# Performance work log

Measured on AMD Instinct MI355X. Metric: run time of the kernel, lower is better.

## Reference

```python
import jax, jax.numpy as jnp
import numpy as np

B, T, I, H = 512, 1024, 64, 128

def setup_inputs() -> dict:
    key = jax.random.key(0)
    ks = jax.random.split(key, 7)
    s_ih = 1.0 / np.sqrt(H)  # torch nn.RNN init scale (uniform +-1/sqrt(H)); use scaled normal for stability
    return {
        "x": jax.random.normal(ks[0], (B, T, I), dtype=jnp.float32),
        "W_ih": jax.random.uniform(ks[1], (H, I), minval=-s_ih, maxval=s_ih, dtype=jnp.float32),
        "W_hh": jax.random.uniform(ks[2], (H, H), minval=-s_ih, maxval=s_ih, dtype=jnp.float32),
        "b_ih": jax.random.uniform(ks[3], (H,), minval=-s_ih, maxval=s_ih, dtype=jnp.float32),
        "b_hh": jax.random.uniform(ks[4], (H,), minval=-s_ih, maxval=s_ih, dtype=jnp.float32),
        "fc_w": jax.random.uniform(ks[5], (1, H), minval=-s_ih, maxval=s_ih, dtype=jnp.float32),
        "fc_b": jax.random.uniform(ks[6], (1,), minval=-s_ih, maxval=s_ih, dtype=jnp.float32),
    }

def reference(x, W_ih, W_hh, b_ih, b_hh, fc_w, fc_b):
    # Precompute input projection for all timesteps in one big GEMM: [B,T,H]
    xp = jnp.einsum("bti,hi->bth", x, W_ih) + b_ih + b_hh
    h0 = jnp.zeros((x.shape[0], W_hh.shape[0]), dtype=x.dtype)

    def step(h, xp_t):
        h = jnp.tanh(xp_t + h @ W_hh.T)
        return h, None

    # scan over time axis; only the final hidden state is needed (out[:, -1, :])
    h_last, _ = jax.lax.scan(step, h0, jnp.swapaxes(xp, 0, 1))
    out = h_last @ fc_w.T + fc_b  # [B, 1]
    return jax.nn.sigmoid(out)
```

## Files before the change

### kernel.cpp

```cpp
#include <hip/hip_runtime.h>


#define Bsz 512
#define Tt  1024
#define Ii  64
#define Hh  128
constexpr int TC = 32;
constexpr int NT = 256;

typedef _Float16 half2v __attribute__((ext_vector_type(2)));
typedef _Float16 half4v __attribute__((ext_vector_type(4)));
typedef _Float16 half8v __attribute__((ext_vector_type(8)));

union h8u { half8v v; half2v h[4]; };

__device__ __forceinline__ float dot2(half2v a, half2v b, float c) {
#if __has_builtin(__builtin_amdgcn_fdot2)
    return __builtin_amdgcn_fdot2(a, b, c, false);
#else
    return c + (float)a[0] * (float)b[0] + (float)a[1] * (float)b[1];
#endif
}

__device__ __forceinline__ float fast_tanh(float x) {
    float t = __builtin_amdgcn_exp2f(x * 2.8853900817779268f);
    return 1.0f - 2.0f * __builtin_amdgcn_rcpf(t + 1.0f);
}
__device__ __forceinline__ float fast_sigmoid(float z) {
    float t = __builtin_amdgcn_exp2f(-z * 1.4426950408889634f);
    return __builtin_amdgcn_rcpf(1.0f + t);
}
__device__ __forceinline__ half4v cvt4(float4 p) {
    half4v r; r[0] = (_Float16)p.x; r[1] = (_Float16)p.y;
    r[2] = (_Float16)p.z; r[3] = (_Float16)p.w; return r;
}

__global__ __launch_bounds__(NT, 4)
void rnn_fused(const float* __restrict__ x,
               const float* __restrict__ W_ih,
               const float* __restrict__ W_hh,
               const float* __restrict__ b_ih,
               const float* __restrict__ b_hh,
               const float* __restrict__ fc_w,
               const float* __restrict__ fc_b,
               float* __restrict__ out)
{
    __shared__ __align__(16) _Float16 xs[2][TC * Ii];
    __shared__ __align__(16) _Float16 hbuf[2][Hh];
    __shared__ float wred[NT / 64];

    const int tid = threadIdx.x;
    const int kq  = tid & 3;
    const int jg  = tid >> 2;
    const int j0  = jg * 2, j1 = j0 + 1;
    const int row = blockIdx.x;

    half2v wih0[8], wih1[8];
    {
        const float* g0 = W_ih + j0 * Ii + kq * 16;
        const float* g1 = W_ih + j1 * Ii + kq * 16;
        #pragma unroll
        for (int k = 0; k < 8; ++k) {
            wih0[k][0] = (_Float16)g0[2*k]; wih0[k][1] = (_Float16)g0[2*k+1];
            wih1[k][0] = (_Float16)g1[2*k]; wih1[k][1] = (_Float16)g1[2*k+1];
        }
    }
    half2v whh0[16], whh1[16];
    {
        const float* g0 = W_hh + j0 * Hh + kq * 32;
        const float* g1 = W_hh + j1 * Hh + kq * 32;
        #pragma unroll
        for (int k = 0; k < 16; ++k) {
            whh0[k][0] = (_Float16)g0[2*k]; whh0[k][1] = (_Float16)g0[2*k+1];
            whh1[k][0] = (_Float16)g1[2*k]; whh1[k][1] = (_Float16)g1[2*k+1];
        }
    }
    const float bias0 = b_ih[j0] + b_hh[j0];
    const float bias1 = b_ih[j1] + b_hh[j1];
    const float fw0 = fc_w[j0], fw1 = fc_w[j1];

    if (tid < Hh / 2) ((half2v*)hbuf[0])[tid] = (half2v)0;

    const float4* xsrc = (const float4*)(x + (size_t)row * Tt * Ii);
    float4 p0 = xsrc[tid];
    float4 p1 = xsrc[tid + NT];

    int   cur = 0;
    float h0n = 0.0f, h1n = 0.0f;

    for (int t0 = 0; t0 < Tt; t0 += TC) {
        const int cbuf = (t0 / TC) & 1;
        ((half4v*)xs[cbuf])[tid]      = cvt4(p0);
        ((half4v*)xs[cbuf])[tid + NT] = cvt4(p1);
        if (t0 + TC < Tt) {
            const int base = (t0 + TC) * (Ii / 4);
            p0 = xsrc[base + tid];
            p1 = xsrc[base + tid + NT];
        }
        __syncthreads();

        #pragma unroll 2
        for (int tt = 0; tt < TC; ++tt) {
            const half8v* xv = (const half8v*)(xs[cbuf] + tt * Ii) + kq * 2;
            const half8v* hv = (const half8v*)(hbuf[cur]) + kq * 4;
            h8u xq0, xq1, hq0, hq1, hq2, hq3;
            xq0.v = xv[0]; xq1.v = xv[1];
            hq0.v = hv[0]; hq1.v = hv[1];
            hq2.v = hv[2]; hq3.v = hv[3];

            float a0 = 0.f, a1 = 0.f, a2 = 0.f, a3 = 0.f;
            float c0 = 0.f, c1 = 0.f, c2 = 0.f, c3 = 0.f;
            #pragma unroll
            for (int k = 0; k < 4; ++k) {
                half2v u0 = xq0.h[k], u1 = xq1.h[k];
                a0 = dot2(u0, wih0[k],     a0);
                a1 = dot2(u1, wih0[k + 4], a1);
                c0 = dot2(u0, wih1[k],     c0);
                c1 = dot2(u1, wih1[k + 4], c1);
            }
            #pragma unroll
            for (int k = 0; k < 4; ++k) {
                half2v v0 = hq0.h[k], v1 = hq1.h[k];
                half2v v2 = hq2.h[k], v3 = hq3.h[k];
                a0 = dot2(v0, whh0[k],      a0);
                a1 = dot2(v1, whh0[k + 4],  a1);
                a2 = dot2(v2, whh0[k + 8],  a2);
                a3 = dot2(v3, whh0[k + 12], a3);
                c0 = dot2(v0, whh1[k],      c0);
                c1 = dot2(v1, whh1[k + 4],  c1);
                c2 = dot2(v2, whh1[k + 8],  c2);
                c3 = dot2(v3, whh1[k + 12], c3);
            }
            float pp0 = (a0 + a1) + (a2 + a3);
            float pp1 = (c0 + c1) + (c2 + c3);
            pp0 += __shfl_xor(pp0, 1, 64);
            pp0 += __shfl_xor(pp0, 2, 64);
            pp1 += __shfl_xor(pp1, 1, 64);
            pp1 += __shfl_xor(pp1, 2, 64);
            h0n = fast_tanh(pp0 + bias0);
            h1n = fast_tanh(pp1 + bias1);
            if (kq == 0) {
                half2v hw; hw[0] = (_Float16)h0n; hw[1] = (_Float16)h1n;
                ((half2v*)hbuf[cur ^ 1])[jg] = hw;
            }
            __syncthreads();
            cur ^= 1;
        }
    }

    float partial = (kq == 0) ? (fw0 * h0n + fw1 * h1n) : 0.0f;
    #pragma unroll
    for (int off = 32; off > 0; off >>= 1)
        partial += __shfl_down(partial, off, 64);
    if ((tid & 63) == 0) wred[tid >> 6] = partial;
    __syncthreads();
    if (tid == 0) {
        float z = fc_b[0];
        #pragma unroll
        for (int w = 0; w < NT / 64; ++w) z += wred[w];
        out[row] = fast_sigmoid(z);
    }
}

extern "C" void kernel_launch(void* const* d_in, const int* in_sizes, int n_in,
                              void* d_out, int out_size, void* d_ws, size_t ws_size,
                              hipStream_t stream) {
    const float* x    = (const float*)d_in[0];
    const float* W_ih = (const float*)d_in[1];
    const float* W_hh = (const float*)d_in[2];
    const float* b_ih = (const float*)d_in[3];
    const float* b_hh = (const float*)d_in[4];
    const float* fc_w = (const float*)d_in[5];
    const float* fc_b = (const float*)d_in[6];
    float* out = (float*)d_out;

    rnn_fused<<<Bsz, NT, 0, stream>>>(x, W_ih, W_hh, b_ih, b_hh, fc_w, fc_b, out);
}
```

Before: 625.5 us.

## Run each batch row's recurrence in a single wavefront without barriers

```diff
diff --git a/kernel.cpp b/kernel.cpp
--- a/kernel.cpp
+++ b/kernel.cpp
@@ -6,7 +6,7 @@
 #define Ii  64
 #define Hh  128
 constexpr int TC = 32;
-constexpr int NT = 256;
+constexpr int NT = 64;
 
 typedef _Float16 half2v __attribute__((ext_vector_type(2)));
 typedef _Float16 half4v __attribute__((ext_vector_type(4)));
@@ -35,42 +35,39 @@
     r[2] = (_Float16)p.z; r[3] = (_Float16)p.w; return r;
 }
 
-__global__ __launch_bounds__(NT, 4)
-void rnn_fused(const float* __restrict__ x,
-               const float* __restrict__ W_ih,
-               const float* __restrict__ W_hh,
-               const float* __restrict__ b_ih,
-               const float* __restrict__ b_hh,
-               const float* __restrict__ fc_w,
-               const float* __restrict__ fc_b,
-               float* __restrict__ out)
+__global__ __launch_bounds__(NT, 1)
+void rnn_wave(const float* __restrict__ x,
+              const float* __restrict__ W_ih,
+              const float* __restrict__ W_hh,
+              const float* __restrict__ b_ih,
+              const float* __restrict__ b_hh,
+              const float* __restrict__ fc_w,
+              const float* __restrict__ fc_b,
+              float* __restrict__ out)
 {
     __shared__ __align__(16) _Float16 xs[2][TC * Ii];
-    __shared__ __align__(16) _Float16 hbuf[2][Hh];
-    __shared__ float wred[NT / 64];
+    __shared__ __align__(16) _Float16 hs[Hh];
 
-    const int tid = threadIdx.x;
-    const int kq  = tid & 3;
-    const int jg  = tid >> 2;
-    const int j0  = jg * 2, j1 = j0 + 1;
+    const int L   = threadIdx.x;
     const int row = blockIdx.x;
+    const int j0  = 2 * L, j1 = j0 + 1;
 
-    half2v wih0[8], wih1[8];
+    half2v wih0[Ii / 2], wih1[Ii / 2];
     {
-        const float* g0 = W_ih + j0 * Ii + kq * 16;
-        const float* g1 = W_ih + j1 * Ii + kq * 16;
+        const float* g0 = W_ih + j0 * Ii;
+        const float* g1 = W_ih + j1 * Ii;
         #pragma unroll
-        for (int k = 0; k < 8; ++k) {
+        for (int k = 0; k < Ii / 2; ++k) {
             wih0[k][0] = (_Float16)g0[2*k]; wih0[k][1] = (_Float16)g0[2*k+1];
             wih1[k][0] = (_Float16)g1[2*k]; wih1[k][1] = (_Float16)g1[2*k+1];
         }
     }
-    half2v whh0[16], whh1[16];
+    half2v whh0[Hh / 2], whh1[Hh / 2];
     {
-        const float* g0 = W_hh + j0 * Hh + kq * 32;
-        const float* g1 = W_hh + j1 * Hh + kq * 32;
+        const float* g0 = W_hh + j0 * Hh;
+        const float* g1 = W_hh + j1 * Hh;
         #pragma unroll
-        for (int k = 0; k < 16; ++k) {
+        for (int k = 0; k < Hh / 2; ++k) {
             whh0[k][0] = (_Float16)g0[2*k]; whh0[k][1] = (_Float16)g0[2*k+1];
             whh1[k][0] = (_Float16)g1[2*k]; whh1[k][1] = (_Float16)g1[2*k+1];
         }
@@ -79,87 +76,70 @@
     const float bias1 = b_ih[j1] + b_hh[j1];
     const float fw0 = fc_w[j0], fw1 = fc_w[j1];
 
-    if (tid < Hh / 2) ((half2v*)hbuf[0])[tid] = (half2v)0;
+    ((half2v*)hs)[L] = (half2v)0;
 
     const float4* xsrc = (const float4*)(x + (size_t)row * Tt * Ii);
-    float4 p0 = xsrc[tid];
-    float4 p1 = xsrc[tid + NT];
+    float4 p[8];
+    #pragma unroll
+    for (int i = 0; i < 8; ++i) p[i] = xsrc[L + 64 * i];
 
-    int   cur = 0;
     float h0n = 0.0f, h1n = 0.0f;
 
     for (int t0 = 0; t0 < Tt; t0 += TC) {
         const int cbuf = (t0 / TC) & 1;
-        ((half4v*)xs[cbuf])[tid]      = cvt4(p0);
-        ((half4v*)xs[cbuf])[tid + NT] = cvt4(p1);
+        #pragma unroll
+        for (int i = 0; i < 8; ++i)
+            ((half4v*)xs[cbuf])[L + 64 * i] = cvt4(p[i]);
         if (t0 + TC < Tt) {
             const int base = (t0 + TC) * (Ii / 4);
-            p0 = xsrc[base + tid];
-            p1 = xsrc[base + tid + NT];
+            #pragma unroll
+            for (int i = 0; i < 8; ++i) p[i] = xsrc[base + L + 64 * i];
         }
-        __syncthreads();
 
-        #pragma unroll 2
+        #pragma unroll 1
         for (int tt = 0; tt < TC; ++tt) {
-            const half8v* xv = (const half8v*)(xs[cbuf] + tt * Ii) + kq * 2;
-            const half8v* hv = (const half8v*)(hbuf[cur]) + kq * 4;
-            h8u xq0, xq1, hq0, hq1, hq2, hq3;
-            xq0.v = xv[0]; xq1.v = xv[1];
-            hq0.v = hv[0]; hq1.v = hv[1];
-            hq2.v = hv[2]; hq3.v = hv[3];
+            const half8v* xv = (const half8v*)(xs[cbuf] + tt * Ii);
+            const half8v* hv = (const half8v*)hs;
 
             float a0 = 0.f, a1 = 0.f, a2 = 0.f, a3 = 0.f;
             float c0 = 0.f, c1 = 0.f, c2 = 0.f, c3 = 0.f;
+
             #pragma unroll
-            for (int k = 0; k < 4; ++k) {
-                half2v u0 = xq0.h[k], u1 = xq1.h[k];
-                a0 = dot2(u0, wih0[k],     a0);
-                a1 = dot2(u1, wih0[k + 4], a1);
-                c0 = dot2(u0, wih1[k],     c0);
-                c1 = dot2(u1, wih1[k + 4], c1);
+            for (int i = 0; i < 8; ++i) {
+                h8u q; q.v = xv[i];
+                a0 = dot2(q.h[0], wih0[4*i+0], a0);
+                a1 = dot2(q.h[1], wih0[4*i+1], a1);
+                a2 = dot2(q.h[2], wih0[4*i+2], a2);
+                a3 = dot2(q.h[3], wih0[4*i+3], a3);
+                c0 = dot2(q.h[0], wih1[4*i+0], c0);
+                c1 = dot2(q.h[1], wih1[4*i+1], c1);
+                c2 = dot2(q.h[2], wih1[4*i+2], c2);
+                c3 = dot2(q.h[3], wih1[4*i+3], c3);
             }
             #pragma unroll
-            for (int k = 0; k < 4; ++k) {
-                half2v v0 = hq0.h[k], v1 = hq1.h[k];
-                half2v v2 = hq2.h[k], v3 = hq3.h[k];
-                a0 = dot2(v0, whh0[k],      a0);
-                a1 = dot2(v1, whh0[k + 4],  a1);
-                a2 = dot2(v2, whh0[k + 8],  a2);
-                a3 = dot2(v3, whh0[k + 12], a3);
-                c0 = dot2(v0, whh1[k],      c0);
-                c1 = dot2(v1, whh1[k + 4],  c1);
-                c2 = dot2(v2, whh1[k + 8],  c2);
-                c3 = dot2(v3, whh1[k + 12], c3);
+            for (int i = 0; i < 16; ++i) {
+                h8u q; q.v = hv[i];
+                a0 = dot2(q.h[0], whh0[4*i+0], a0);
+                a1 = dot2(q.h[1], whh0[4*i+1], a1);
+                a2 = dot2(q.h[2], whh0[4*i+2], a2);
+                a3 = dot2(q.h[3], whh0[4*i+3], a3);
+                c0 = dot2(q.h[0], whh1[4*i+0], c0);
+                c1 = dot2(q.h[1], whh1[4*i+1], c1);
+                c2 = dot2(q.h[2], whh1[4*i+2], c2);
+                c3 = dot2(q.h[3], whh1[4*i+3], c3);
             }
-            float pp0 = (a0 + a1) + (a2 + a3);
-            float pp1 = (c0 + c1) + (c2 + c3);
-            pp0 += __shfl_xor(pp0, 1, 64);
-            pp0 += __shfl_xor(pp0, 2, 64);
-            pp1 += __shfl_xor(pp1, 1, 64);
-            pp1 += __shfl_xor(pp1, 2, 64);
-            h0n = fast_tanh(pp0 + bias0);
-            h1n = fast_tanh(pp1 + bias1);
-            if (kq == 0) {
-                half2v hw; hw[0] = (_Float16)h0n; hw[1] = (_Float16)h1n;
-                ((half2v*)hbuf[cur ^ 1])[jg] = hw;
-            }
-            __syncthreads();
-            cur ^= 1;
+            h0n = fast_tanh(((a0 + a1) + (a2 + a3)) + bias0);
+            h1n = fast_tanh(((c0 + c1) + (c2 + c3)) + bias1);
+            half2v hw; hw[0] = (_Float16)h0n; hw[1] = (_Float16)h1n;
+            ((half2v*)hs)[L] = hw;
         }
     }
 
-    float partial = (kq == 0) ? (fw0 * h0n + fw1 * h1n) : 0.0f;
+    float partial = fw0 * h0n + fw1 * h1n;
     #pragma unroll
     for (int off = 32; off > 0; off >>= 1)
         partial += __shfl_down(partial, off, 64);
-    if ((tid & 63) == 0) wred[tid >> 6] = partial;
-    __syncthreads();
-    if (tid == 0) {
-        float z = fc_b[0];
-        #pragma unroll
-        for (int w = 0; w < NT / 64; ++w) z += wred[w];
-        out[row] = fast_sigmoid(z);
-    }
+    if (L == 0) out[row] = fast_sigmoid(partial + fc_b[0]);
 }
 
 extern "C" void kernel_launch(void* const* d_in, const int* in_sizes, int n_in,
@@ -174,5 +154,5 @@
     const float* fc_b = (const float*)d_in[6];
     float* out = (float*)d_out;
 
-    rnn_fused<<<Bsz, NT, 0, stream>>>(x, W_ih, W_hh, b_ih, b_hh, fc_w, fc_b, out);
+    rnn_wave<<<Bsz, NT, 0, stream>>>(x, W_ih, W_hh, b_ih, b_hh, fc_w, fc_b, out);
 }
```

Result: slower. 1.120 ms (+79.1%).
